# Optimization experiments

Measured on AMD Instinct MI355X. Metric: run time of the kernel, lower is better.

The kernel has to match this reference:

```python
import jax, jax.numpy as jnp
import numpy as np

B, S, D, H, L, V, DF = 2, 1024, 1024, 16, 4, 32000, 4096


def setup_inputs() -> dict:
    key = jax.random.key(0)
    ks = iter(jax.random.split(key, 64))
    rn = lambda shape, s=0.02: jax.random.normal(next(ks), shape, jnp.float32) * s
    inp = {
        'dec_input': rn((B, S, D), 1.0),
        'enc_input': rn((B, S, D), 1.0),
        # additive masks: causal for self-attn, none for cross-attn
        'masked_attention_mask': jnp.where(jnp.tril(jnp.ones((S, S), bool)), 0.0, -1e9)[None, None].astype(jnp.float32),
        'cross_attention_mask': jnp.zeros((1, 1, S, S), jnp.float32),
        'num_heads': H,
    }
    for p in ['sWq', 'sWk', 'sWv', 'sWo', 'cWq', 'cWk', 'cWv', 'cWo']:
        inp[p] = rn((L, D, D))
    for p in ['sbq', 'sbk', 'sbv', 'sbo', 'cbq', 'cbk', 'cbv', 'cbo']:
        inp[p] = jnp.zeros((L, D), jnp.float32)
    for p in ['ln1_g', 'ln2_g', 'ln3_g']:
        inp[p] = jnp.ones((L, D), jnp.float32)
    for p in ['ln1_b', 'ln2_b', 'ln3_b']:
        inp[p] = jnp.zeros((L, D), jnp.float32)
    inp['fW1'] = rn((L, D, DF)); inp['fb1'] = jnp.zeros((L, DF), jnp.float32)
    inp['fW2'] = rn((L, DF, D)); inp['fb2'] = jnp.zeros((L, D), jnp.float32)
    inp['Wout'] = rn((D, V)); inp['bout'] = jnp.zeros((V,), jnp.float32)
    return inp


def positional_encoding(seq_len, d_model, n=10000.0):
    # vectorized equivalent of the original triple-nested loop:
    # even d -> sin(i / n^(d/D)); odd d -> cos(i / n^((d-1)/D)); d==0 denom 1 == n^0
    i = jnp.arange(seq_len, dtype=jnp.float32)[:, None]
    d = jnp.arange(d_model)
    denom = jnp.power(n, (2 * (d // 2)).astype(jnp.float32) / d_model)
    ang = i / denom
    return jnp.where(d % 2 == 0, jnp.sin(ang), jnp.cos(ang))  # [S, D]


def layer_norm(x, g, b, eps=1e-5):
    m = jnp.mean(x, -1, keepdims=True)
    v = jnp.mean(jnp.square(x - m), -1, keepdims=True)
    return (x - m) * jax.lax.rsqrt(v + eps) * g + b


def mha(q_in, k_in, v_in, mask, Wq, bq, Wk, bk, Wv, bv, Wo, bo, h):
    b, sq, d = q_in.shape
    dh = d // h
    q = (q_in @ Wq + bq).reshape(b, sq, h, dh)
    k = (k_in @ Wk + bk).reshape(b, -1, h, dh)
    v = (v_in @ Wv + bv).reshape(b, -1, h, dh)
    scores = jnp.einsum('bqhd,bkhd->bhqk', q, k) / jnp.sqrt(jnp.float32(dh)) + mask
    attn = jax.nn.softmax(scores, axis=-1)
    out = jnp.einsum('bhqk,bkhd->bqhd', attn, v).reshape(b, sq, d)
    return out @ Wo + bo


def reference(dec_input, enc_input, masked_attention_mask, cross_attention_mask,
              sWq, sbq, sWk, sbk, sWv, sbv, sWo, sbo,
              cWq, cbq, cWk, cbk, cWv, cbv, cWo, cbo,
              ln1_g, ln1_b, ln2_g, ln2_b, ln3_g, ln3_b,
              fW1, fb1, fW2, fb2, Wout, bout, num_heads):
    b, s, d = dec_input.shape
    x0 = dec_input + positional_encoding(s, d)
    n_layers = sWq.shape[0]
    y = x0
    for l in range(n_layers):
        # NOTE: original DecoderSequential bug: every block consumes the ORIGINAL input;
        # only the last block's output survives.
        a1 = layer_norm(x0 + mha(x0, x0, x0, masked_attention_mask,
                                 sWq[l], sbq[l], sWk[l], sbk[l], sWv[l], sbv[l], sWo[l], sbo[l], num_heads),
                        ln1_g[l], ln1_b[l])
        a2 = layer_norm(a1 + mha(a1, enc_input, enc_input, cross_attention_mask,
                                 cWq[l], cbq[l], cWk[l], cbk[l], cWv[l], cbv[l], cWo[l], cbo[l], num_heads),
                        ln2_g[l], ln2_b[l])
        ff = jax.nn.relu(a2 @ fW1[l] + fb1[l]) @ fW2[l] + fb2[l]
        y = layer_norm(a2 + ff, ln3_g[l], ln3_b[l])
    return y @ Wout + bout  # [B, S, V]
```

## Files before the change

### kernel.cpp

```cpp
#include <hip/hip_runtime.h>
#include <cstdint>
#include <cstddef>

#define DEV __device__ __forceinline__

typedef __attribute__((ext_vector_type(8))) short short8;
typedef __attribute__((ext_vector_type(4))) float f32x4;
typedef __attribute__((ext_vector_type(4))) unsigned short ushort4v;

DEV unsigned short f2bf(float f){
  union { float f; unsigned int i; } v; v.f = f;
  unsigned int r = v.i + 0x7fffu + ((v.i >> 16) & 1u);
  return (unsigned short)(r >> 16);
}

DEV void gld_lds16(const unsigned short* g, unsigned short* lds){
  __builtin_amdgcn_global_load_lds((const __attribute__((address_space(1))) void*)g,
                                   (__attribute__((address_space(3))) void*)lds, 16, 0, 0);
}

template<int BM, int BN, int EPI>
__global__ __launch_bounds__(256, 2)
void gemm_bt(const unsigned short* __restrict__ A,
             const unsigned short* __restrict__ Bt,
             const float* __restrict__ bias,
             void* __restrict__ C, int M, int N, int K)
{
  constexpr int MF = BM / 32, NF = BN / 32;
  constexpr int LA = BM / 64, LB = BN / 64;
  __shared__ __align__(16) unsigned short lds[2 * (BM + BN) * 32];

  const int tid = threadIdx.x, w = tid >> 6, l = tid & 63;
  const int wr = w >> 1, wc = w & 1;

  const int nbm = M / BM, nbn = N / BN;
  const int nwg = nbm * nbn;
  const int q8 = nwg >> 3, r8 = nwg & 7;
  const int xcd = blockIdx.x & 7, within = blockIdx.x >> 3;
  const int wg = (xcd < r8 ? xcd * (q8 + 1) : r8 * (q8 + 1) + (xcd - r8) * q8) + within;
  const int mb = (wg % nbm) * BM, nb = (wg / nbm) * BN;

  unsigned short* As0 = lds;
  unsigned short* Bs0 = lds + BM * 32;
  unsigned short* As1 = lds + (BM + BN) * 32;
  unsigned short* Bs1 = As1 + BM * 32;

  f32x4 acc[MF][NF];
  #pragma unroll
  for (int m = 0; m < MF; m++)
    #pragma unroll
    for (int n = 0; n < NF; n++) acc[m][n] = (f32x4){0.f, 0.f, 0.f, 0.f};

  const int srow = l >> 2;
  const int scol = (((l & 3) ^ ((l >> 2) & 3) ^ ((l >> 4) & 3)) * 8);
  const int rswz = (l & 3) ^ ((l >> 2) & 3);

  #define STAGE(Ad, Bd, k0) do { \
    _Pragma("unroll") \
    for (int i = 0; i < LA; i++){ \
      int chunk = i * 4 + w; \
      gld_lds16(A + (size_t)(mb + chunk * 16 + srow) * K + (k0) + scol, (Ad) + chunk * 512); \
    } \
    _Pragma("unroll") \
    for (int i = 0; i < LB; i++){ \
      int chunk = i * 4 + w; \
      gld_lds16(Bt + (size_t)(nb + chunk * 16 + srow) * K + (k0) + scol, (Bd) + chunk * 512); \
    } } while(0)

  STAGE(As0, Bs0, 0);
  const int nk = K / 32;
  const int rdoff = ((l >> 4) ^ rswz) * 8;
  for (int kt = 0; kt < nk; kt++){
    __syncthreads();
    unsigned short* Ac = (kt & 1) ? As1 : As0;
    unsigned short* Bc = (kt & 1) ? Bs1 : Bs0;
    if (kt + 1 < nk){
      unsigned short* An = (kt & 1) ? As0 : As1;
      unsigned short* Bn = (kt & 1) ? Bs0 : Bs1;
      STAGE(An, Bn, (kt + 1) * 32);
    }
    short8 af[MF], bfr[NF];
    #pragma unroll
    for (int m = 0; m < MF; m++)
      af[m] = *(const short8*)(Ac + (wr * (BM / 2) + m * 16 + (l & 15)) * 32 + rdoff);
    #pragma unroll
    for (int n = 0; n < NF; n++)
      bfr[n] = *(const short8*)(Bc + (wc * (BN / 2) + n * 16 + (l & 15)) * 32 + rdoff);
    #pragma unroll
    for (int m = 0; m < MF; m++)
      #pragma unroll
      for (int n = 0; n < NF; n++)
        acc[m][n] = __builtin_amdgcn_mfma_f32_16x16x32_bf16(af[m], bfr[n], acc[m][n], 0, 0, 0);
  }
  #undef STAGE

  #pragma unroll
  for (int n = 0; n < NF; n++){
    const int col = nb + wc * (BN / 2) + n * 16 + (l & 15);
    const float bv = bias ? bias[col] : 0.f;
    #pragma unroll
    for (int m = 0; m < MF; m++){
      const int row0 = mb + wr * (BM / 2) + m * 16 + ((l >> 4) << 2);
      #pragma unroll
      for (int jj = 0; jj < 4; jj++){
        float v = acc[m][n][jj] + bv;
        size_t idx = (size_t)(row0 + jj) * N + col;
        if (EPI == 0)       ((float*)C)[idx] = v;
        else if (EPI == 3)  __builtin_nontemporal_store(v, &((float*)C)[idx]);
        else if (EPI == 1)  ((unsigned short*)C)[idx] = f2bf(v);
        else { v = v > 0.f ? v : 0.f; ((unsigned short*)C)[idx] = f2bf(v); }
      }
    }
  }
}

template<int CAUSAL>
__global__ __launch_bounds__(256)
void attn_kernel(const unsigned short* __restrict__ Qb, int ldq,
                 const unsigned short* __restrict__ Kb, int ldk,
                 const unsigned short* __restrict__ Vb, int ldv,
                 unsigned short* __restrict__ Ob, int ldo)
{
  constexpr int S = 1024;
  __shared__ __align__(16) unsigned short vt[64][40];
  __shared__ __align__(16) unsigned short plds[4][16][40];
  const int tid = threadIdx.x, w = tid >> 6, l = tid & 63;
  const int qt = blockIdx.x, bh = blockIdx.y;
  const int b = bh >> 4, h = bh & 15;
  const int hoff = h * 64;
  const size_t rb = (size_t)b * S;

  const int qrow = qt * 64 + w * 16 + (l & 15);
  const unsigned short* qp = Qb + (rb + qrow) * ldq + hoff + ((l >> 4) * 8);
  short8 qf0 = *(const short8*)qp;
  short8 qf1 = *(const short8*)(qp + 32);

  float m_run[4] = {-1e30f, -1e30f, -1e30f, -1e30f};
  float l_run[4] = {0.f, 0.f, 0.f, 0.f};
  f32x4 oacc[4];
  #pragma unroll
  for (int t = 0; t < 4; t++) oacc[t] = (f32x4){0.f, 0.f, 0.f, 0.f};

  const int qmax = qt * 64 + w * 16 + 15;
  const int nkeys = CAUSAL ? (qt * 64 + 64) : S;
  const int skey = tid >> 3, sd8 = (tid & 7) * 8;

  for (int kb = 0; kb < nkeys; kb += 32){
    short8 vv = *(const short8*)(Vb + (rb + kb + skey) * ldv + hoff + sd8);
    #pragma unroll
    for (int i = 0; i < 8; i++) vt[sd8 + i][skey] = (unsigned short)vv[i];
    __syncthreads();
    if (!CAUSAL || kb <= qmax){
      f32x4 sc[2];
      #pragma unroll
      for (int g = 0; g < 2; g++){
        const unsigned short* kp = Kb + (rb + kb + g * 16 + (l & 15)) * ldk + hoff + ((l >> 4) * 8);
        short8 kf0 = *(const short8*)kp;
        short8 kf1 = *(const short8*)(kp + 32);
        f32x4 z = (f32x4){0.f, 0.f, 0.f, 0.f};
        z = __builtin_amdgcn_mfma_f32_16x16x32_bf16(qf0, kf0, z, 0, 0, 0);
        z = __builtin_amdgcn_mfma_f32_16x16x32_bf16(qf1, kf1, z, 0, 0, 0);
        sc[g] = z;
      }
      #pragma unroll
      for (int jj = 0; jj < 4; jj++){
        float s0 = sc[0][jj] * 0.125f, s1 = sc[1][jj] * 0.125f;
        if (CAUSAL){
          int q = qt * 64 + w * 16 + ((l >> 4) << 2) + jj;
          if (kb + (l & 15) > q)      s0 = -1e30f;
          if (kb + 16 + (l & 15) > q) s1 = -1e30f;
        }
        float mx = fmaxf(s0, s1);
        mx = fmaxf(mx, __shfl_xor(mx, 1));
        mx = fmaxf(mx, __shfl_xor(mx, 2));
        mx = fmaxf(mx, __shfl_xor(mx, 4));
        mx = fmaxf(mx, __shfl_xor(mx, 8));
        float mnew = fmaxf(m_run[jj], mx);
        float scal = __expf(m_run[jj] - mnew);
        m_run[jj] = mnew;
        float p0 = __expf(s0 - mnew), p1 = __expf(s1 - mnew);
        float rs = p0 + p1;
        rs += __shfl_xor(rs, 1); rs += __shfl_xor(rs, 2);
        rs += __shfl_xor(rs, 4); rs += __shfl_xor(rs, 8);
        l_run[jj] = l_run[jj] * scal + rs;
        #pragma unroll
        for (int t = 0; t < 4; t++) oacc[t][jj] *= scal;
        int qr = ((l >> 4) << 2) + jj;
        plds[w][qr][l & 15]      = f2bf(p0);
        plds[w][qr][16 + (l & 15)] = f2bf(p1);
      }
      asm volatile("s_waitcnt lgkmcnt(0)" ::: "memory");
      short8 pf = *(const short8*)&plds[w][l & 15][(l >> 4) * 8];
      #pragma unroll
      for (int t = 0; t < 4; t++){
        short8 vf = *(const short8*)&vt[t * 16 + (l & 15)][(l >> 4) * 8];
        oacc[t] = __builtin_amdgcn_mfma_f32_16x16x32_bf16(pf, vf, oacc[t], 0, 0, 0);
      }
    }
    __syncthreads();
  }
  #pragma unroll
  for (int jj = 0; jj < 4; jj++){
    float inv = 1.f / l_run[jj];
    int q = qt * 64 + w * 16 + ((l >> 4) << 2) + jj;
    #pragma unroll
    for (int t = 0; t < 4; t++)
      Ob[(rb + q) * ldo + hoff + t * 16 + (l & 15)] = f2bf(oacc[t][jj] * inv);
  }
}

__global__ __launch_bounds__(256)
void ln_kernel(const float* __restrict__ x1, const float* __restrict__ x2,
               const float* __restrict__ g, const float* __restrict__ be,
               float* __restrict__ outf, unsigned short* __restrict__ outb)
{
  const int row = blockIdx.x, t = threadIdx.x;
  __shared__ float red[4];
  const float4 v1 = ((const float4*)(x1 + (size_t)row * 1024))[t];
  const float4 v2 = ((const float4*)(x2 + (size_t)row * 1024))[t];
  float x[4] = {v1.x + v2.x, v1.y + v2.y, v1.z + v2.z, v1.w + v2.w};
  float s = x[0] + x[1] + x[2] + x[3];
  for (int o = 1; o < 64; o <<= 1) s += __shfl_xor(s, o);
  const int w = t >> 6, l = t & 63;
  if (l == 0) red[w] = s;
  __syncthreads();
  const float mean = (red[0] + red[1] + red[2] + red[3]) * (1.f / 1024.f);
  float d[4]; float sq = 0.f;
  #pragma unroll
  for (int i = 0; i < 4; i++){ d[i] = x[i] - mean; sq += d[i] * d[i]; }
  __syncthreads();
  for (int o = 1; o < 64; o <<= 1) sq += __shfl_xor(sq, o);
  if (l == 0) red[w] = sq;
  __syncthreads();
  const float var = (red[0] + red[1] + red[2] + red[3]) * (1.f / 1024.f);
  const float inv = rsqrtf(var + 1e-5f);
  const int base = t * 4;
  #pragma unroll
  for (int i = 0; i < 4; i++){
    float o = d[i] * inv * g[base + i] + be[base + i];
    if (outf) outf[(size_t)row * 1024 + base + i] = o;
    outb[(size_t)row * 1024 + base + i] = f2bf(o);
  }
}

__global__ __launch_bounds__(256)
void build_x0(const float* __restrict__ dec, float* __restrict__ xf, unsigned short* __restrict__ xb)
{
  const int i = blockIdx.x * 256 + threadIdx.x;
  const int i4 = i * 4;
  const int d0 = i4 & 1023;
  const int s  = (i4 >> 10) & 1023;
  float4 dv = ((const float4*)dec)[i];
  const float* dvp = (const float*)&dv;
  float o[4];
  #pragma unroll
  for (int j = 0; j < 4; j++){
    int dd = d0 + j;
    float e = (float)(dd & ~1) * (1.f / 1024.f);
    float den = expf(e * 9.210340371976184f);
    float ang = (float)s / den;
    float pe = (dd & 1) ? cosf(ang) : sinf(ang);
    o[j] = dvp[j] + pe;
  }
  ((float4*)xf)[i] = make_float4(o[0], o[1], o[2], o[3]);
  ushort4v ob; ob[0] = f2bf(o[0]); ob[1] = f2bf(o[1]); ob[2] = f2bf(o[2]); ob[3] = f2bf(o[3]);
  ((ushort4v*)xb)[i] = ob;
}

__global__ __launch_bounds__(256)
void cvt_bf16_k(const float* __restrict__ in, unsigned short* __restrict__ out)
{
  const int i = blockIdx.x * 256 + threadIdx.x;
  float4 v = ((const float4*)in)[i];
  ushort4v o; o[0] = f2bf(v.x); o[1] = f2bf(v.y); o[2] = f2bf(v.z); o[3] = f2bf(v.w);
  ((ushort4v*)out)[i] = o;
}

__global__ __launch_bounds__(256)
void transpose_cvt(const float* __restrict__ in, unsigned short* __restrict__ out, int R, int C)
{
  __shared__ float t[32][33];
  const int cb = blockIdx.x * 32, rbk = blockIdx.y * 32;
  const int tx = threadIdx.x & 31, ty = threadIdx.x >> 5;
  #pragma unroll
  for (int i = 0; i < 4; i++)
    t[ty + 8 * i][tx] = in[(size_t)(rbk + ty + 8 * i) * C + cb + tx];
  __syncthreads();
  #pragma unroll
  for (int i = 0; i < 4; i++){
    int c = ty + 8 * i;
    out[(size_t)(cb + c) * R + rbk + tx] = f2bf(t[tx][c]);
  }
}

struct TPtrs { const float* src[8]; unsigned short* dst[8]; };
__global__ __launch_bounds__(256)
void transpose_cvt8(TPtrs p)
{
  __shared__ float t[32][33];
  const float* __restrict__ in = p.src[blockIdx.z];
  unsigned short* __restrict__ out = p.dst[blockIdx.z];
  const int cb = blockIdx.x * 32, rbk = blockIdx.y * 32;
  const int tx = threadIdx.x & 31, ty = threadIdx.x >> 5;
  #pragma unroll
  for (int i = 0; i < 4; i++)
    t[ty + 8 * i][tx] = in[(size_t)(rbk + ty + 8 * i) * 1024 + cb + tx];
  __syncthreads();
  #pragma unroll
  for (int i = 0; i < 4; i++){
    int c = ty + 8 * i;
    out[(size_t)(cb + c) * 1024 + rbk + tx] = f2bf(t[tx][c]);
  }
}

__global__ __launch_bounds__(256)
void copy_biases(const float* sbq, const float* sbk, const float* sbv,
                 const float* cbk, const float* cbv,
                 float* bqkv, float* bkvc)
{
  const int i = blockIdx.x * 256 + threadIdx.x;
  const int seg = i >> 10, off = i & 1023;
  if (seg == 0)      bqkv[off] = sbq[off];
  else if (seg == 1) bqkv[1024 + off] = sbk[off];
  else if (seg == 2) bqkv[2048 + off] = sbv[off];
  else if (seg == 3) bkvc[off] = cbk[off];
  else               bkvc[1024 + off] = cbv[off];
}

extern "C" void kernel_launch(void* const* d_in, const int* in_sizes, int n_in,
                              void* d_out, int out_size, void* d_ws, size_t ws_size,
                              hipStream_t stream)
{
  constexpr int S = 1024, D = 1024, V = 32000, DF = 4096;
  constexpr int M = 2 * S;
  constexpr int DD = D * D;
  constexpr int l3 = 3;

  const float* dec  = (const float*)d_in[0];
  const float* enc  = (const float*)d_in[1];
  const float* sWq = (const float*)d_in[5]  + l3 * DD;
  const float* sWk = (const float*)d_in[6]  + l3 * DD;
  const float* sWv = (const float*)d_in[7]  + l3 * DD;
  const float* sWo = (const float*)d_in[8]  + l3 * DD;
  const float* cWq = (const float*)d_in[9]  + l3 * DD;
  const float* cWk = (const float*)d_in[10] + l3 * DD;
  const float* cWv = (const float*)d_in[11] + l3 * DD;
  const float* cWo = (const float*)d_in[12] + l3 * DD;
  const float* sbq = (const float*)d_in[13] + l3 * D;
  const float* sbk = (const float*)d_in[14] + l3 * D;
  const float* sbv = (const float*)d_in[15] + l3 * D;
  const float* sbo = (const float*)d_in[16] + l3 * D;
  const float* cbq = (const float*)d_in[17] + l3 * D;
  const float* cbk = (const float*)d_in[18] + l3 * D;
  const float* cbv = (const float*)d_in[19] + l3 * D;
  const float* cbo = (const float*)d_in[20] + l3 * D;
  const float* ln1g = (const float*)d_in[21] + l3 * D;
  const float* ln2g = (const float*)d_in[22] + l3 * D;
  const float* ln3g = (const float*)d_in[23] + l3 * D;
  const float* ln1b = (const float*)d_in[24] + l3 * D;
  const float* ln2b = (const float*)d_in[25] + l3 * D;
  const float* ln3b = (const float*)d_in[26] + l3 * D;
  const float* fW1 = (const float*)d_in[27] + (size_t)l3 * D * DF;
  const float* fb1 = (const float*)d_in[28] + l3 * DF;
  const float* fW2 = (const float*)d_in[29] + (size_t)l3 * DF * D;
  const float* fb2 = (const float*)d_in[30] + l3 * D;
  const float* Wout = (const float*)d_in[31];
  const float* bout = (const float*)d_in[32];
  float* out = (float*)d_out;

  uint8_t* wsp = (uint8_t*)d_ws;
  auto alloc = [&](size_t bytes) -> void* {
    void* p = wsp; wsp += (bytes + 255) & ~(size_t)255; return p;
  };
  float*          x0f  = (float*)alloc((size_t)M * D * 4);
  unsigned short* x0b  = (unsigned short*)alloc((size_t)M * D * 2);
  unsigned short* encb = (unsigned short*)alloc((size_t)M * D * 2);
  unsigned short* wqkv = (unsigned short*)alloc((size_t)3 * DD * 2);
  unsigned short* wos  = (unsigned short*)alloc((size_t)DD * 2);
  unsigned short* wqc  = (unsigned short*)alloc((size_t)DD * 2);
  unsigned short* wkvc = (unsigned short*)alloc((size_t)2 * DD * 2);
  unsigned short* woc  = (unsigned short*)alloc((size_t)DD * 2);
  unsigned short* wf1  = (unsigned short*)alloc((size_t)D * DF * 2);
  unsigned short* wf2  = (unsigned short*)alloc((size_t)D * DF * 2);
  unsigned short* wvo  = (unsigned short*)alloc((size_t)V * D * 2);
  float*          bqkv = (float*)alloc(3 * D * 4);
  float*          bkvc = (float*)alloc(2 * D * 4);
  unsigned short* qkv  = (unsigned short*)alloc((size_t)M * 3 * D * 2);
  unsigned short* attnb= (unsigned short*)alloc((size_t)M * D * 2);
  float*          oproj= (float*)alloc((size_t)M * D * 4);
  float*          a1f  = (float*)alloc((size_t)M * D * 4);
  unsigned short* a1b  = (unsigned short*)alloc((size_t)M * D * 2);
  unsigned short* qc   = (unsigned short*)alloc((size_t)M * D * 2);
  unsigned short* kvc  = (unsigned short*)alloc((size_t)M * 2 * D * 2);
  float*          a2f  = (float*)alloc((size_t)M * D * 4);
  unsigned short* a2b  = (unsigned short*)alloc((size_t)M * D * 2);
  unsigned short* ffh  = (unsigned short*)alloc((size_t)M * DF * 2);
  unsigned short* yb   = (unsigned short*)alloc((size_t)M * D * 2);

  build_x0<<<M * D / 4 / 256, 256, 0, stream>>>(dec, x0f, x0b);
  cvt_bf16_k<<<M * D / 4 / 256, 256, 0, stream>>>(enc, encb);

  TPtrs tp;
  tp.src[0] = sWq; tp.dst[0] = wqkv;
  tp.src[1] = sWk; tp.dst[1] = wqkv + DD;
  tp.src[2] = sWv; tp.dst[2] = wqkv + 2 * DD;
  tp.src[3] = sWo; tp.dst[3] = wos;
  tp.src[4] = cWq; tp.dst[4] = wqc;
  tp.src[5] = cWk; tp.dst[5] = wkvc;
  tp.src[6] = cWv; tp.dst[6] = wkvc + DD;
  tp.src[7] = cWo; tp.dst[7] = woc;
  transpose_cvt8<<<dim3(32, 32, 8), 256, 0, stream>>>(tp);
  transpose_cvt<<<dim3(DF/32, D/32), 256, 0, stream>>>(fW1, wf1, D, DF);
  transpose_cvt<<<dim3(D/32, DF/32), 256, 0, stream>>>(fW2, wf2, DF, D);
  transpose_cvt<<<dim3(V/32, D/32), 256, 0, stream>>>(Wout, wvo, D, V);
  copy_biases<<<20, 256, 0, stream>>>(sbq, sbk, sbv, cbk, cbv, bqkv, bkvc);

  gemm_bt<64,128,1><<<(M/64)*(3*D/128), 256, 0, stream>>>(x0b, wqkv, bqkv, qkv, M, 3*D, D);
  attn_kernel<1><<<dim3(S/64, 32), 256, 0, stream>>>(qkv, 3*D, qkv + D, 3*D, qkv + 2*D, 3*D, attnb, D);
  gemm_bt<64,64,0><<<(M/64)*(D/64), 256, 0, stream>>>(attnb, wos, sbo, oproj, M, D, D);
  ln_kernel<<<M, 256, 0, stream>>>(x0f, oproj, ln1g, ln1b, a1f, a1b);

  gemm_bt<64,64,1><<<(M/64)*(D/64), 256, 0, stream>>>(a1b, wqc, cbq, qc, M, D, D);
  gemm_bt<64,128,1><<<(M/64)*(2*D/128), 256, 0, stream>>>(encb, wkvc, bkvc, kvc, M, 2*D, D);
  attn_kernel<0><<<dim3(S/64, 32), 256, 0, stream>>>(qc, D, kvc, 2*D, kvc + D, 2*D, attnb, D);
  gemm_bt<64,64,0><<<(M/64)*(D/64), 256, 0, stream>>>(attnb, woc, cbo, oproj, M, D, D);
  ln_kernel<<<M, 256, 0, stream>>>(a1f, oproj, ln2g, ln2b, a2f, a2b);

  gemm_bt<128,128,2><<<(M/128)*(DF/128), 256, 0, stream>>>(a2b, wf1, fb1, ffh, M, DF, D);
  gemm_bt<64,64,0><<<(M/64)*(D/64), 256, 0, stream>>>(ffh, wf2, fb2, oproj, M, D, DF);
  ln_kernel<<<M, 256, 0, stream>>>(a2f, oproj, ln3g, ln3b, nullptr, yb);

  gemm_bt<128,128,3><<<(M/128)*(V/128), 256, 0, stream>>>(yb, wvo, bout, out, M, V, D);
}
```

Before: 650.5 us.

## Add 256x256 eight-wave pipelined GEMM for FFN1 and vocab projection

Adds a new GEMM kernel with 256x256 output tiles, 512 threads and double-buffered LDS staging via direct global-to-LDS loads. Loads for the next k-step are interleaved with four MFMA phases per step. It replaces the 128x128 GEMM for the FFN up-projection and the large vocabulary projection, aiming at more operand reuse per byte loaded. The FFN down-projection tile also grows from 64x64 to 64x128. The 128KB LDS footprint limits occupancy to one block per CU, and FFN1 drops to only 128 workgroups, which may underfill the GPU.

After: 662.3 us. No clear change (+1.8%).

```diff
diff --git a/kernel.cpp b/kernel.cpp
--- a/kernel.cpp
+++ b/kernel.cpp
@@ -17,6 +17,127 @@
 DEV void gld_lds16(const unsigned short* g, unsigned short* lds){
   __builtin_amdgcn_global_load_lds((const __attribute__((address_space(1))) void*)g,
                                    (__attribute__((address_space(3))) void*)lds, 16, 0, 0);
+}
+
+template<int EPI>
+__global__ __launch_bounds__(512, 2)
+void gemm256(const unsigned short* __restrict__ A,
+             const unsigned short* __restrict__ Bt,
+             const float* __restrict__ bias,
+             void* __restrict__ C, int M, int N, int K)
+{
+  __shared__ __align__(16) unsigned short lds[65536];
+
+  const int tid = threadIdx.x, wid = tid >> 6, l = tid & 63;
+  const int wr = wid >> 2, wc = wid & 3;
+
+  const int nbm = M / 256, nbn = N / 256;
+  const int nwg = nbm * nbn;
+  const int q8 = nwg >> 3, r8 = nwg & 7;
+  const int xcd = blockIdx.x & 7, within = blockIdx.x >> 3;
+  const int wg = (xcd < r8 ? xcd * (q8 + 1) : r8 * (q8 + 1) + (xcd - r8) * q8) + within;
+  const int mb = (wg % nbm) * 256, nb = (wg / nbm) * 256;
+
+  const int nk = K / 64;
+
+  const int srow8 = tid >> 3;
+  const int sslot = (tid & 7) ^ ((tid >> 3) & 7);
+
+  const int rl = l & 15, kslot = l >> 4, sx = l & 7;
+  const int so0 = ((kslot) ^ sx) * 8;
+  const int so1 = ((4 + kslot) ^ sx) * 8;
+  const int arowb = wr * 128 + rl;
+  const int bline = wc * 32 + rl;
+
+  f32x4 acc[8][4];
+  #pragma unroll
+  for (int m = 0; m < 8; m++)
+    #pragma unroll
+    for (int n = 0; n < 4; n++) acc[m][n] = (f32x4){0.f, 0.f, 0.f, 0.f};
+
+#define STAGE_A(c, tt, pp) \
+  gld_lds16(A + (size_t)(mb + (c)*64 + srow8) * K + (size_t)(tt)*64 + sslot*8, \
+            lds + (pp)*32768 + (c)*4096 + tid*8)
+#define STAGE_B(c, tt, pp) \
+  gld_lds16(Bt + (size_t)(nb + (((c)*2 + (srow8>>5)) & 3)*64 + ((c)>>1)*32 + (srow8&31)) * K \
+                 + (size_t)(tt)*64 + sslot*8, \
+            lds + (pp)*32768 + 16384 + (c)*4096 + tid*8)
+
+#define PHASE(mh, nh, STAGES, TAIL) do { \
+    short8 af[4][2], bf[2][2]; \
+    _Pragma("unroll") \
+    for (int i = 0; i < 4; i++){ \
+      const unsigned short* ap = lds + pof + (arowb + (mh)*64 + i*16) * 64; \
+      af[i][0] = *(const short8*)(ap + so0); \
+      af[i][1] = *(const short8*)(ap + so1); \
+    } \
+    _Pragma("unroll") \
+    for (int j = 0; j < 2; j++){ \
+      const unsigned short* bp = lds + pof + 16384 + ((nh)*128 + bline + j*16) * 64; \
+      bf[j][0] = *(const short8*)(bp + so0); \
+      bf[j][1] = *(const short8*)(bp + so1); \
+    } \
+    STAGES; \
+    asm volatile("" ::: "memory"); \
+    __builtin_amdgcn_s_barrier(); \
+    asm volatile("s_waitcnt lgkmcnt(0)" ::: "memory"); \
+    __builtin_amdgcn_s_setprio(1); \
+    _Pragma("unroll") \
+    for (int i = 0; i < 4; i++) \
+      _Pragma("unroll") \
+      for (int j = 0; j < 2; j++){ \
+        acc[(mh)*4+i][(nh)*2+j] = __builtin_amdgcn_mfma_f32_16x16x32_bf16(af[i][0], bf[j][0], acc[(mh)*4+i][(nh)*2+j], 0, 0, 0); \
+        acc[(mh)*4+i][(nh)*2+j] = __builtin_amdgcn_mfma_f32_16x16x32_bf16(af[i][1], bf[j][1], acc[(mh)*4+i][(nh)*2+j], 0, 0, 0); \
+      } \
+    __builtin_amdgcn_s_setprio(0); \
+    TAIL; \
+    asm volatile("" ::: "memory"); \
+    __builtin_amdgcn_s_barrier(); \
+  } while(0)
+
+  STAGE_A(0, 0, 0); STAGE_A(1, 0, 0); STAGE_A(2, 0, 0); STAGE_A(3, 0, 0);
+  STAGE_B(0, 0, 0); STAGE_B(1, 0, 0); STAGE_B(2, 0, 0); STAGE_B(3, 0, 0);
+  if (nk > 1){ STAGE_B(0, 1, 1); STAGE_B(1, 1, 1); STAGE_A(0, 1, 1); STAGE_A(2, 1, 1); }
+  if (nk > 1) asm volatile("s_waitcnt vmcnt(4)" ::: "memory");
+  else        asm volatile("s_waitcnt vmcnt(0)" ::: "memory");
+  asm volatile("" ::: "memory");
+  __builtin_amdgcn_s_barrier();
+
+  int pcur = 0;
+  for (int u = 0; u < nk; u++){
+    const int pof = pcur * 32768;
+    const int pnx = pcur ^ 1;
+    const bool s1 = (u + 1 < nk), s2 = (u + 2 < nk);
+    PHASE(0, 0, { if (s1){ STAGE_B(2, u + 1, pnx); STAGE_B(3, u + 1, pnx); } }, {});
+    PHASE(1, 0, { if (s1){ STAGE_A(1, u + 1, pnx); STAGE_A(3, u + 1, pnx); } }, {});
+    PHASE(0, 1, { if (s2){ STAGE_B(0, u + 2, pcur); STAGE_B(1, u + 2, pcur); } }, {});
+    PHASE(1, 1, { if (s2){ STAGE_A(0, u + 2, pcur); STAGE_A(2, u + 2, pcur); } },
+          { if (u == nk - 2)     asm volatile("s_waitcnt vmcnt(0)" ::: "memory");
+            else if (u < nk - 2) asm volatile("s_waitcnt vmcnt(4)" ::: "memory"); });
+    pcur ^= 1;
+  }
+#undef PHASE
+#undef STAGE_A
+#undef STAGE_B
+
+  #pragma unroll
+  for (int n = 0; n < 4; n++){
+    const int col = nb + wc * 64 + n * 16 + rl;
+    const float bv = bias ? bias[col] : 0.f;
+    #pragma unroll
+    for (int m = 0; m < 8; m++){
+      const int row0 = mb + wr * 128 + m * 16 + (kslot << 2);
+      #pragma unroll
+      for (int jj = 0; jj < 4; jj++){
+        float v = acc[m][n][jj] + bv;
+        size_t idx = (size_t)(row0 + jj) * N + col;
+        if (EPI == 0)       ((float*)C)[idx] = v;
+        else if (EPI == 3)  __builtin_nontemporal_store(v, &((float*)C)[idx]);
+        else if (EPI == 1)  ((unsigned short*)C)[idx] = f2bf(v);
+        else { v = v > 0.f ? v : 0.f; ((unsigned short*)C)[idx] = f2bf(v); }
+      }
+    }
+  }
 }
 
 template<int BM, int BN, int EPI>
@@ -426,9 +547,9 @@
   gemm_bt<64,64,0><<<(M/64)*(D/64), 256, 0, stream>>>(attnb, woc, cbo, oproj, M, D, D);
   ln_kernel<<<M, 256, 0, stream>>>(a1f, oproj, ln2g, ln2b, a2f, a2b);
 
-  gemm_bt<128,128,2><<<(M/128)*(DF/128), 256, 0, stream>>>(a2b, wf1, fb1, ffh, M, DF, D);
-  gemm_bt<64,64,0><<<(M/64)*(D/64), 256, 0, stream>>>(ffh, wf2, fb2, oproj, M, D, DF);
+  gemm256<2><<<(M/256)*(DF/256), 512, 0, stream>>>(a2b, wf1, fb1, ffh, M, DF, D);
+  gemm_bt<64,128,0><<<(M/64)*(D/128), 256, 0, stream>>>(ffh, wf2, fb2, oproj, M, D, DF);
   ln_kernel<<<M, 256, 0, stream>>>(a2f, oproj, ln3g, ln3b, nullptr, yb);
 
-  gemm_bt<128,128,3><<<(M/128)*(V/128), 256, 0, stream>>>(yb, wvo, bout, out, M, V, D);
-}
+  gemm256<3><<<(M/256)*(V/256), 512, 0, stream>>>(yb, wvo, bout, out, M, V, D);
+}
```

## Add 512-thread 128x128 GEMM with split-phase LDS pipelining for large projections

Applied to the files above, without the earlier changes.

Adds a new 8-wave 128x128 GEMM kernel that splits each K-step into two half-tile phases. Each phase overlaps global-to-LDS loads of the next tile with MFMA work and raises wave priority around the MFMA blocks. It replaces the QKV, cross-KV, FFN1 and vocab-projection GEMMs. The FFN2 GEMM also moves to a 64x128 tile. The aim is more waves per CU and better hiding of load latency, at the cost of more barriers per K-step and higher LDS use per block.

New measurement: 647.4 us. About the same (-0.5%).

```diff
diff --git a/kernel.cpp b/kernel.cpp
--- a/kernel.cpp
+++ b/kernel.cpp
@@ -17,6 +17,134 @@
 DEV void gld_lds16(const unsigned short* g, unsigned short* lds){
   __builtin_amdgcn_global_load_lds((const __attribute__((address_space(1))) void*)g,
                                    (__attribute__((address_space(3))) void*)lds, 16, 0, 0);
+}
+
+template<int EPI>
+__global__ __launch_bounds__(512, 4)
+void gemm128p(const unsigned short* __restrict__ A,
+              const unsigned short* __restrict__ Bt,
+              const float* __restrict__ bias,
+              void* __restrict__ C, int M, int N, int K)
+{
+  __shared__ __align__(16) unsigned short lds[32768];
+
+  const int tid = threadIdx.x, wid = tid >> 6, l = tid & 63;
+  const int wr = wid >> 2, wc = wid & 3;
+
+  const int nbm = M / 128, nbn = N / 128;
+  const int nwg = nbm * nbn;
+  const int q8 = nwg >> 3, r8 = nwg & 7;
+  const int xcd = blockIdx.x & 7, within = blockIdx.x >> 3;
+  const int wg = (xcd < r8 ? xcd * (q8 + 1) : r8 * (q8 + 1) + (xcd - r8) * q8) + within;
+  const int mb = (wg % nbm) * 128, nb = (wg / nbm) * 128;
+
+  const int nk = K / 64;
+
+  const int sA_row = (tid >> 8) * 64 + ((tid >> 3) & 31);
+  const int sB_row = tid >> 3;
+  const int scol = ((tid & 7) ^ ((tid >> 3) & 7)) * 8;
+
+  const int rl = l & 15, kg = l >> 4;
+  const int so0 = ((kg)     ^ (l & 7)) * 8;
+  const int so1 = ((4 + kg) ^ (l & 7)) * 8;
+
+  f32x4 acc[4][2];
+  #pragma unroll
+  for (int m = 0; m < 4; m++)
+    #pragma unroll
+    for (int n = 0; n < 2; n++) acc[m][n] = (f32x4){0.f, 0.f, 0.f, 0.f};
+
+#define STAGE_A(i, tt, pp) \
+  gld_lds16(A + (size_t)(mb + sA_row + (i)*32) * K + (size_t)(tt)*64 + scol, \
+            lds + (pp)*16384 + (i)*4096 + tid*8)
+#define STAGE_B(i, tt, pp) \
+  gld_lds16(Bt + (size_t)(nb + (i)*64 + sB_row) * K + (size_t)(tt)*64 + scol, \
+            lds + (pp)*16384 + 8192 + (i)*4096 + tid*8)
+#define BAR() do { asm volatile("" ::: "memory"); __builtin_amdgcn_s_barrier(); \
+                   asm volatile("" ::: "memory"); } while(0)
+
+  STAGE_B(0, 0, 0); STAGE_B(1, 0, 0); STAGE_A(0, 0, 0); STAGE_A(1, 0, 0);
+  asm volatile("s_waitcnt vmcnt(1)" ::: "memory");
+  BAR();
+
+  for (int u = 0; u < nk; u++){
+    const int p = u & 1;
+    const unsigned short* buf = lds + p * 16384;
+    const unsigned short* bB  = buf + 8192 + (wc * 32 + rl) * 64;
+    short8 bfr[2][2], af[2][2];
+
+    #pragma unroll
+    for (int n = 0; n < 2; n++){
+      bfr[n][0] = *(const short8*)(bB + n * 1024 + so0);
+      bfr[n][1] = *(const short8*)(bB + n * 1024 + so1);
+    }
+    {
+      const unsigned short* aB = buf + (wr * 32 + rl) * 64;
+      #pragma unroll
+      for (int f = 0; f < 2; f++){
+        af[f][0] = *(const short8*)(aB + f * 1024 + so0);
+        af[f][1] = *(const short8*)(aB + f * 1024 + so1);
+      }
+    }
+    if (u + 1 < nk){ STAGE_B(0, u + 1, p ^ 1); STAGE_B(1, u + 1, p ^ 1); }
+    BAR();
+    __builtin_amdgcn_s_setprio(1);
+    #pragma unroll
+    for (int f = 0; f < 2; f++)
+      #pragma unroll
+      for (int n = 0; n < 2; n++){
+        acc[f][n] = __builtin_amdgcn_mfma_f32_16x16x32_bf16(af[f][0], bfr[n][0], acc[f][n], 0, 0, 0);
+        acc[f][n] = __builtin_amdgcn_mfma_f32_16x16x32_bf16(af[f][1], bfr[n][1], acc[f][n], 0, 0, 0);
+      }
+    __builtin_amdgcn_s_setprio(0);
+    if (u + 1 < nk) asm volatile("s_waitcnt vmcnt(2)" ::: "memory");
+    else            asm volatile("s_waitcnt vmcnt(0)" ::: "memory");
+    BAR();
+
+    {
+      const unsigned short* aB = buf + 4096 + (wr * 32 + rl) * 64;
+      #pragma unroll
+      for (int f = 0; f < 2; f++){
+        af[f][0] = *(const short8*)(aB + f * 1024 + so0);
+        af[f][1] = *(const short8*)(aB + f * 1024 + so1);
+      }
+    }
+    if (u + 1 < nk){ STAGE_A(0, u + 1, p ^ 1); STAGE_A(1, u + 1, p ^ 1); }
+    BAR();
+    __builtin_amdgcn_s_setprio(1);
+    #pragma unroll
+    for (int f = 0; f < 2; f++)
+      #pragma unroll
+      for (int n = 0; n < 2; n++){
+        acc[2 + f][n] = __builtin_amdgcn_mfma_f32_16x16x32_bf16(af[f][0], bfr[n][0], acc[2 + f][n], 0, 0, 0);
+        acc[2 + f][n] = __builtin_amdgcn_mfma_f32_16x16x32_bf16(af[f][1], bfr[n][1], acc[2 + f][n], 0, 0, 0);
+      }
+    __builtin_amdgcn_s_setprio(0);
+    if (u + 1 < nk) asm volatile("s_waitcnt vmcnt(1)" ::: "memory");
+    BAR();
+  }
+#undef BAR
+#undef STAGE_A
+#undef STAGE_B
+
+  #pragma unroll
+  for (int n = 0; n < 2; n++){
+    const int col = nb + wc * 32 + n * 16 + rl;
+    const float bv = bias ? bias[col] : 0.f;
+    #pragma unroll
+    for (int m = 0; m < 4; m++){
+      const int row0 = mb + wr * 64 + m * 16 + kg * 4;
+      #pragma unroll
+      for (int jj = 0; jj < 4; jj++){
+        float v = acc[m][n][jj] + bv;
+        size_t idx = (size_t)(row0 + jj) * N + col;
+        if (EPI == 0)       ((float*)C)[idx] = v;
+        else if (EPI == 3)  __builtin_nontemporal_store(v, &((float*)C)[idx]);
+        else if (EPI == 1)  ((unsigned short*)C)[idx] = f2bf(v);
+        else { v = v > 0.f ? v : 0.f; ((unsigned short*)C)[idx] = f2bf(v); }
+      }
+    }
+  }
 }
 
 template<int BM, int BN, int EPI>
@@ -415,20 +543,20 @@
   transpose_cvt<<<dim3(V/32, D/32), 256, 0, stream>>>(Wout, wvo, D, V);
   copy_biases<<<20, 256, 0, stream>>>(sbq, sbk, sbv, cbk, cbv, bqkv, bkvc);
 
-  gemm_bt<64,128,1><<<(M/64)*(3*D/128), 256, 0, stream>>>(x0b, wqkv, bqkv, qkv, M, 3*D, D);
+  gemm128p<1><<<(M/128)*(3*D/128), 512, 0, stream>>>(x0b, wqkv, bqkv, qkv, M, 3*D, D);
   attn_kernel<1><<<dim3(S/64, 32), 256, 0, stream>>>(qkv, 3*D, qkv + D, 3*D, qkv + 2*D, 3*D, attnb, D);
   gemm_bt<64,64,0><<<(M/64)*(D/64), 256, 0, stream>>>(attnb, wos, sbo, oproj, M, D, D);
   ln_kernel<<<M, 256, 0, stream>>>(x0f, oproj, ln1g, ln1b, a1f, a1b);
 
   gemm_bt<64,64,1><<<(M/64)*(D/64), 256, 0, stream>>>(a1b, wqc, cbq, qc, M, D, D);
-  gemm_bt<64,128,1><<<(M/64)*(2*D/128), 256, 0, stream>>>(encb, wkvc, bkvc, kvc, M, 2*D, D);
+  gemm128p<1><<<(M/128)*(2*D/128), 512, 0, stream>>>(encb, wkvc, bkvc, kvc, M, 2*D, D);
   attn_kernel<0><<<dim3(S/64, 32), 256, 0, stream>>>(qc, D, kvc, 2*D, kvc + D, 2*D, attnb, D);
   gemm_bt<64,64,0><<<(M/64)*(D/64), 256, 0, stream>>>(attnb, woc, cbo, oproj, M, D, D);
   ln_kernel<<<M, 256, 0, stream>>>(a1f, oproj, ln2g, ln2b, a2f, a2b);
 
-  gemm_bt<128,128,2><<<(M/128)*(DF/128), 256, 0, stream>>>(a2b, wf1, fb1, ffh, M, DF, D);
-  gemm_bt<64,64,0><<<(M/64)*(D/64), 256, 0, stream>>>(ffh, wf2, fb2, oproj, M, D, DF);
+  gemm128p<2><<<(M/128)*(DF/128), 512, 0, stream>>>(a2b, wf1, fb1, ffh, M, DF, D);
+  gemm_bt<64,128,0><<<(M/64)*(D/128), 256, 0, stream>>>(ffh, wf2, fb2, oproj, M, D, DF);
   ln_kernel<<<M, 256, 0, stream>>>(a2f, oproj, ln3g, ln3b, nullptr, yb);
 
-  gemm_bt<128,128,3><<<(M/128)*(V/128), 256, 0, stream>>>(yb, wvo, bout, out, M, V, D);
-}
+  gemm128p<3><<<(M/128)*(V/128), 512, 0, stream>>>(yb, wvo, bout, out, M, V, D);
+}
```

## Add 32x32x16 MFMA GEMM with triple-buffered LDS for large projections

Applied to the files above, without the earlier changes.

Adds a new GEMM kernel built on 32x32x16 bf16 MFMA instructions. It uses a three-stage LDS ring with global_load_lds prefetch two K-steps ahead, interleaves the loads with compute, and raises wave priority around the MFMA blocks. It replaces the QKV, cross KV, FFN1 and vocabulary projection GEMMs, using 128x256 tiles for the vocabulary projection. The FFN2 tile also changes to 64x128. The larger tiles and accumulators increase register pressure and may reduce occupancy or wave count on the smaller GEMMs.

Measured after the change: 623.7 us. 1.04x faster.

```diff
diff --git a/kernel.cpp b/kernel.cpp
--- a/kernel.cpp
+++ b/kernel.cpp
@@ -6,6 +6,7 @@
 
 typedef __attribute__((ext_vector_type(8))) short short8;
 typedef __attribute__((ext_vector_type(4))) float f32x4;
+typedef __attribute__((ext_vector_type(16))) float f32x16;
 typedef __attribute__((ext_vector_type(4))) unsigned short ushort4v;
 
 DEV unsigned short f2bf(float f){
@@ -17,6 +18,140 @@
 DEV void gld_lds16(const unsigned short* g, unsigned short* lds){
   __builtin_amdgcn_global_load_lds((const __attribute__((address_space(1))) void*)g,
                                    (__attribute__((address_space(3))) void*)lds, 16, 0, 0);
+}
+
+template<int BN, int EPI>
+__global__ __launch_bounds__(256, 2)
+void gemm32(const unsigned short* __restrict__ A,
+            const unsigned short* __restrict__ Bt,
+            const float* __restrict__ bias,
+            void* __restrict__ C, int M, int N, int K)
+{
+  constexpr int NFR  = BN / 64;
+  constexpr int ROWS = 128 + BN;
+  constexpr int BUFH = ROWS * 32;
+  constexpr int GLD  = ROWS / 64;
+  __shared__ __align__(16) unsigned short lds[3 * BUFH];
+
+  const int tid = threadIdx.x, wid = tid >> 6, l = tid & 63;
+  const int wr = wid >> 1, wcn = wid & 1;
+
+  const int nbm = M / 128, nbn = N / BN;
+  const int nwg = nbm * nbn;
+  const int q8 = nwg >> 3, r8 = nwg & 7;
+  const int xcd = blockIdx.x & 7, within = blockIdx.x >> 3;
+  const int wg = (xcd < r8 ? xcd * (q8 + 1) : r8 * (q8 + 1) + (xcd - r8) * q8) + within;
+  const int mb = (wg % nbm) * 128, nb = (wg / nbm) * BN;
+
+  const int nk = K / 32;
+
+  const int r31 = l & 31, hi = l >> 5;
+  const int so0 = (( hi)      ^ (r31 & 3)) * 8;
+  const int so1 = ((2 + hi)   ^ (r31 & 3)) * 8;
+  const int abase = (wr * 64 + r31) * 32;
+  const int bbase = 4096 + (wcn * (BN / 2) + r31) * 32;
+
+  f32x16 acc[2][NFR];
+  #pragma unroll
+  for (int m = 0; m < 2; m++)
+    #pragma unroll
+    for (int n = 0; n < NFR; n++)
+      #pragma unroll
+      for (int e = 0; e < 16; e++) acc[m][n][e] = 0.f;
+
+#define STAGE_A(c, tt, bb) \
+  gld_lds16(A + (size_t)(mb + (c)*64 + (tid>>2)) * K + (size_t)(tt)*32 + (((tid&3)^((tid>>2)&3))*8), \
+            lds + (bb)*BUFH + (c)*2048 + tid*8)
+#define STAGE_B(c, tt, bb) \
+  gld_lds16(Bt + (size_t)(nb + (c)*64 + (tid>>2)) * K + (size_t)(tt)*32 + (((tid&3)^((tid>>2)&3))*8), \
+            lds + (bb)*BUFH + 4096 + (c)*2048 + tid*8)
+#define WAIT_GLD() do { if constexpr (GLD == 6) asm volatile("s_waitcnt vmcnt(6)" ::: "memory"); \
+                        else                    asm volatile("s_waitcnt vmcnt(4)" ::: "memory"); } while(0)
+
+  STAGE_A(0, 0, 0); STAGE_A(1, 0, 0);
+  #pragma unroll
+  for (int c = 0; c < NFR; c++) STAGE_B(c, 0, 0);
+  if (nk > 1){
+    STAGE_A(0, 1, 1); STAGE_A(1, 1, 1);
+    #pragma unroll
+    for (int c = 0; c < NFR; c++) STAGE_B(c, 1, 1);
+    WAIT_GLD();
+  } else {
+    asm volatile("s_waitcnt vmcnt(0)" ::: "memory");
+  }
+  asm volatile("" ::: "memory");
+  __builtin_amdgcn_s_barrier();
+  asm volatile("" ::: "memory");
+
+  int bb = 0;
+  for (int u = 0; u < nk; u++){
+    const unsigned short* buf = lds + bb * BUFH;
+    const int sb = (bb >= 1) ? bb - 1 : 2;
+    const bool st = (u + 2 < nk);
+    short8 af[2], bf[NFR];
+
+    af[0] = *(const short8*)(buf + abase + so0);
+    af[1] = *(const short8*)(buf + abase + 1024 + so0);
+    #pragma unroll
+    for (int n = 0; n < NFR; n++) bf[n] = *(const short8*)(buf + bbase + n * 1024 + so0);
+    if (st){
+      STAGE_A(0, u + 2, sb); STAGE_A(1, u + 2, sb);
+      if constexpr (NFR == 4) STAGE_B(0, u + 2, sb);
+    }
+    __builtin_amdgcn_s_setprio(1);
+    #pragma unroll
+    for (int m = 0; m < 2; m++)
+      #pragma unroll
+      for (int n = 0; n < NFR; n++)
+        acc[m][n] = __builtin_amdgcn_mfma_f32_32x32x16_bf16(af[m], bf[n], acc[m][n], 0, 0, 0);
+    __builtin_amdgcn_s_setprio(0);
+
+    af[0] = *(const short8*)(buf + abase + so1);
+    af[1] = *(const short8*)(buf + abase + 1024 + so1);
+    #pragma unroll
+    for (int n = 0; n < NFR; n++) bf[n] = *(const short8*)(buf + bbase + n * 1024 + so1);
+    if (st){
+      if constexpr (NFR == 4){ STAGE_B(1, u + 2, sb); STAGE_B(2, u + 2, sb); STAGE_B(3, u + 2, sb); }
+      else                   { STAGE_B(0, u + 2, sb); STAGE_B(1, u + 2, sb); }
+    }
+    __builtin_amdgcn_s_setprio(1);
+    #pragma unroll
+    for (int m = 0; m < 2; m++)
+      #pragma unroll
+      for (int n = 0; n < NFR; n++)
+        acc[m][n] = __builtin_amdgcn_mfma_f32_32x32x16_bf16(af[m], bf[n], acc[m][n], 0, 0, 0);
+    __builtin_amdgcn_s_setprio(0);
+
+    if (st)               WAIT_GLD();
+    else if (u + 1 < nk)  asm volatile("s_waitcnt vmcnt(0)" ::: "memory");
+    asm volatile("" ::: "memory");
+    __builtin_amdgcn_s_barrier();
+    asm volatile("" ::: "memory");
+    bb = (bb == 2) ? 0 : bb + 1;
+  }
+#undef WAIT_GLD
+#undef STAGE_A
+#undef STAGE_B
+
+  #pragma unroll
+  for (int n = 0; n < NFR; n++){
+    const int col = nb + wcn * (BN / 2) + n * 32 + r31;
+    const float bv = bias ? bias[col] : 0.f;
+    #pragma unroll
+    for (int m = 0; m < 2; m++){
+      const int rowb = mb + wr * 64 + m * 32 + 4 * hi;
+      #pragma unroll
+      for (int reg = 0; reg < 16; reg++){
+        const int row = rowb + (reg & 3) + 8 * (reg >> 2);
+        float v = acc[m][n][reg] + bv;
+        size_t idx = (size_t)row * N + col;
+        if (EPI == 0)       ((float*)C)[idx] = v;
+        else if (EPI == 3)  __builtin_nontemporal_store(v, &((float*)C)[idx]);
+        else if (EPI == 1)  ((unsigned short*)C)[idx] = f2bf(v);
+        else { v = v > 0.f ? v : 0.f; ((unsigned short*)C)[idx] = f2bf(v); }
+      }
+    }
+  }
 }
 
 template<int BM, int BN, int EPI>
@@ -415,20 +550,20 @@
   transpose_cvt<<<dim3(V/32, D/32), 256, 0, stream>>>(Wout, wvo, D, V);
   copy_biases<<<20, 256, 0, stream>>>(sbq, sbk, sbv, cbk, cbv, bqkv, bkvc);
 
-  gemm_bt<64,128,1><<<(M/64)*(3*D/128), 256, 0, stream>>>(x0b, wqkv, bqkv, qkv, M, 3*D, D);
+  gemm32<128,1><<<(M/128)*(3*D/128), 256, 0, stream>>>(x0b, wqkv, bqkv, qkv, M, 3*D, D);
   attn_kernel<1><<<dim3(S/64, 32), 256, 0, stream>>>(qkv, 3*D, qkv + D, 3*D, qkv + 2*D, 3*D, attnb, D);
   gemm_bt<64,64,0><<<(M/64)*(D/64), 256, 0, stream>>>(attnb, wos, sbo, oproj, M, D, D);
   ln_kernel<<<M, 256, 0, stream>>>(x0f, oproj, ln1g, ln1b, a1f, a1b);
 
   gemm_bt<64,64,1><<<(M/64)*(D/64), 256, 0, stream>>>(a1b, wqc, cbq, qc, M, D, D);
-  gemm_bt<64,128,1><<<(M/64)*(2*D/128), 256, 0, stream>>>(encb, wkvc, bkvc, kvc, M, 2*D, D);
+  gemm32<128,1><<<(M/128)*(2*D/128), 256, 0, stream>>>(encb, wkvc, bkvc, kvc, M, 2*D, D);
   attn_kernel<0><<<dim3(S/64, 32), 256, 0, stream>>>(qc, D, kvc, 2*D, kvc + D, 2*D, attnb, D);
   gemm_bt<64,64,0><<<(M/64)*(D/64), 256, 0, stream>>>(attnb, woc, cbo, oproj, M, D, D);
   ln_kernel<<<M, 256, 0, stream>>>(a1f, oproj, ln2g, ln2b, a2f, a2b);
 
-  gemm_bt<128,128,2><<<(M/128)*(DF/128), 256, 0, stream>>>(a2b, wf1, fb1, ffh, M, DF, D);
-  gemm_bt<64,64,0><<<(M/64)*(D/64), 256, 0, stream>>>(ffh, wf2, fb2, oproj, M, D, DF);
+  gemm32<128,2><<<(M/128)*(DF/128), 256, 0, stream>>>(a2b, wf1, fb1, ffh, M, DF, D);
+  gemm_bt<64,128,0><<<(M/64)*(D/128), 256, 0, stream>>>(ffh, wf2, fb2, oproj, M, D, DF);
   ln_kernel<<<M, 256, 0, stream>>>(a2f, oproj, ln3g, ln3b, nullptr, yb);
 
-  gemm_bt<128,128,3><<<(M/128)*(V/128), 256, 0, stream>>>(yb, wvo, bout, out, M, V, D);
-}
+  gemm32<256,3><<<(M/128)*(V/256), 256, 0, stream>>>(yb, wvo, bout, out, M, V, D);
+}
```
